# Kernel tuning notes

Hardware: AMD Instinct MI355X
Metric: run time of the kernel (lower is better)

## Reference

```python
import jax, jax.numpy as jnp
import numpy as np

DIM = 512; H = 8; KH = 2; G = 4; DH = 64        # dim, q heads, kv heads, GQA group, head dim
BALL = 128; SEL = 64; TOPK = 2; PDIM = 3        # sliding ball, compress/selection block, topk, pos dim
SCALE = DH ** -0.5


def _rms_norm(x, gamma):
    return x * jax.lax.rsqrt(jnp.mean(x * x, axis=-1, keepdims=True) + 1e-6) * gamma


def _rotary(t):
    # t: (B, h, S, DH); GPT-NeoX style rotate-half rotary embedding
    S = t.shape[-2]
    inv = 1.0 / (10000.0 ** (jnp.arange(0, DH, 2, dtype=jnp.float32) / DH))
    f = jnp.arange(S, dtype=jnp.float32)[:, None] * inv          # (S, DH/2)
    cos = jnp.concatenate([jnp.cos(f), jnp.cos(f)], -1)
    sin = jnp.concatenate([jnp.sin(f), jnp.sin(f)], -1)
    t1, t2 = jnp.split(t, 2, -1)
    return t * cos + jnp.concatenate([-t2, t1], -1) * sin


def _forward(x, pos, pe_w, pe_b, gamma, wq, wk, wv, k_pos, v_pos,
             k_w1, k_b1, k_w2, k_b2, v_w1, v_b1, v_w2, v_b2,
             mem_k, mem_v, w_combine, w_out, num_batches):
    B = num_batches
    # relative position of leaves wrt ball center (no-grad in original)
    p = jax.lax.stop_gradient(pos).reshape(-1, SEL, PDIM)
    rel = (p - p.mean(axis=1, keepdims=True)).reshape(-1, PDIM)
    x = x + rel @ pe_w + pe_b
    x = x.reshape(B, -1, DIM)
    S = x.shape[1]
    nb = S // SEL
    h = _rms_norm(x, gamma)
    q = (h @ wq).reshape(B, S, H, DH).transpose(0, 2, 1, 3)      # (B,H,S,DH)
    k = (h @ wk).reshape(B, S, KH, DH).transpose(0, 2, 1, 3)     # (B,KH,S,DH)
    v = (h @ wv).reshape(B, S, KH, DH).transpose(0, 2, 1, 3)
    qr, kr = _rotary(q), _rotary(k)

    # --- compressed branch: per-block intra-pos emb + MLP compression ---
    kb = k.reshape(B, KH, nb, SEL, DH) + k_pos[None, :, None]
    vb = v.reshape(B, KH, nb, SEL, DH) + v_pos[None, :, None]
    ck = jax.nn.relu(kb.reshape(B, KH, nb, SEL * DH) @ k_w1 + k_b1) @ k_w2 + k_b2
    cv = jax.nn.relu(vb.reshape(B, KH, nb, SEL * DH) @ v_w1 + v_b1) @ v_w2 + v_b2
    ck = jnp.concatenate([jnp.broadcast_to(mem_k[None], (B, KH, 1, DH)), ck], axis=2)
    cv = jnp.concatenate([jnp.broadcast_to(mem_v[None], (B, KH, 1, DH)), cv], axis=2)
    qg = qr.reshape(B, KH, G, S, DH)
    csim = jnp.einsum('bkgsd,bknd->bkgsn', qg, ck) * SCALE
    cattn = jax.nn.softmax(csim, axis=-1)
    cout = jnp.einsum('bkgsn,bknd->bkgsd', cattn, cv).reshape(B, H, S, DH)

    # --- top-k block selection from compressed attention importance ---
    imp = cattn[..., 1:].mean(axis=2)                            # share over grouped q heads: (B,KH,S,nb)
    imp_blk = imp.reshape(B, KH, nb, SEL, nb).mean(axis=3)       # per query block: (B,KH,nb,nb)
    _, sel = jax.lax.top_k(imp_blk, TOPK)                        # (B,KH,nb,TOPK)

    # --- fine branch: each query block attends own + TOPK selected blocks ---
    kblk = kr.reshape(B, KH, nb, SEL, DH)
    vblk = v.reshape(B, KH, nb, SEL, DH)
    gather = jax.vmap(jax.vmap(lambda t, s: t[s]))               # (nb,SEL,DH),(nb,TOPK)->(nb,TOPK,SEL,DH)
    fk = jnp.concatenate([gather(kblk, sel), kblk[:, :, :, None]], axis=3)
    fv = jnp.concatenate([gather(vblk, sel), vblk[:, :, :, None]], axis=3)
    fk = fk.reshape(B, KH, nb, (TOPK + 1) * SEL, DH)
    fv = fv.reshape(B, KH, nb, (TOPK + 1) * SEL, DH)
    qb = qr.reshape(B, KH, G, nb, SEL, DH)
    fsim = jnp.einsum('bkgnqd,bknmd->bkgnqm', qb, fk) * SCALE
    fout = jnp.einsum('bkgnqm,bknmd->bkgnqd', jax.nn.softmax(fsim, -1), fv)
    fout = fout.reshape(B, H, S, DH)

    # --- sliding branch: MiniBallAttn = plain SDPA within balls of size 128 ---
    nw = S // BALL
    qw = qr.reshape(B, H, nw, BALL, DH)
    kw = jnp.repeat(kr, G, axis=1).reshape(B, H, nw, BALL, DH)
    vw = jnp.repeat(v, G, axis=1).reshape(B, H, nw, BALL, DH)
    ssim = jnp.einsum('bhnqd,bhnkd->bhnqk', qw, kw) * SCALE
    sout = jnp.einsum('bhnqk,bhnkd->bhnqd', jax.nn.softmax(ssim, -1), vw)
    sout = sout.reshape(B, H, S, DH)

    # --- sigmoid-gated strategy combine, merge heads, out projection ---
    gates = jax.nn.sigmoid(h @ w_combine).reshape(B, S, H, 3).transpose(0, 2, 1, 3)
    out = gates[..., 0:1] * cout + gates[..., 1:2] * fout + gates[..., 2:3] * sout
    out = out.transpose(0, 2, 1, 3).reshape(B, S, H * DH) @ w_out
    return out.reshape(-1, DIM)


def setup_inputs() -> dict:
    key = jax.random.key(0)
    ks = jax.random.split(key, 16)
    Bn, S = 8, 4096
    N = Bn * S
    CD = SEL * DH
    def lin(k, fi, fo):
        return (jax.random.normal(k, (fi, fo), jnp.float32) / np.sqrt(fi)).astype(jnp.float32)
    return {
        'x': jax.random.normal(ks[0], (N, DIM), jnp.float32),
        'pos': jax.random.normal(ks[1], (N, PDIM), jnp.float32),
        'pe_w': lin(ks[2], PDIM, DIM),
        'pe_b': jnp.zeros((DIM,), jnp.float32),
        'gamma': jnp.ones((DIM,), jnp.float32),
        'wq': lin(ks[3], DIM, H * DH),
        'wk': lin(ks[4], DIM, KH * DH),
        'wv': lin(ks[5], DIM, KH * DH),
        'k_pos': jax.random.normal(ks[6], (KH, SEL, DH), jnp.float32) * 0.02,
        'v_pos': jax.random.normal(ks[7], (KH, SEL, DH), jnp.float32) * 0.02,
        'k_w1': lin(ks[8], CD, CD), 'k_b1': jnp.zeros((CD,), jnp.float32),
        'k_w2': lin(ks[9], CD, DH), 'k_b2': jnp.zeros((DH,), jnp.float32),
        'v_w1': lin(ks[10], CD, CD), 'v_b1': jnp.zeros((CD,), jnp.float32),
        'v_w2': lin(ks[11], CD, DH), 'v_b2': jnp.zeros((DH,), jnp.float32),
        'mem_k': jax.random.normal(ks[12], (KH, 1, DH), jnp.float32) * 0.02,
        'mem_v': jax.random.normal(ks[13], (KH, 1, DH), jnp.float32) * 0.02,
        'w_combine': lin(ks[14], DIM, 3 * H),
        'w_out': lin(ks[15], H * DH, DIM),
        'num_batches': 8,
    }


def reference(x, pos, pe_w, pe_b, gamma, wq, wk, wv, k_pos, v_pos,
              k_w1, k_b1, k_w2, k_b2, v_w1, v_b1, v_w2, v_b2,
              mem_k, mem_v, w_combine, w_out, num_batches):
    return _forward(x, pos, pe_w, pe_b, gamma, wq, wk, wv, k_pos, v_pos,
                    k_w1, k_b1, k_w2, k_b2, v_w1, v_b1, v_w2, v_b2,
                    mem_k, mem_v, w_combine, w_out, num_batches)
```

## Files before the change

kernel.cpp:

```cpp
#include <hip/hip_runtime.h>
#include <stdint.h>

#define DEVI static __device__ __forceinline__
typedef unsigned short u16;
typedef __bf16 bhalf8 __attribute__((ext_vector_type(8)));
typedef float f32x4 __attribute__((ext_vector_type(4)));

DEVI u16 f2bf(float f) {
  union { float f; unsigned u; } v; v.f = f;
  unsigned r = v.u + 0x7FFFu + ((v.u >> 16) & 1u);
  return (u16)(r >> 16);
}
DEVI float bf2f(u16 h) {
  union { unsigned u; float f; } v; v.u = ((unsigned)h) << 16;
  return v.f;
}
DEVI f32x4 MFMA(bhalf8 a, bhalf8 b, f32x4 c) {
  return __builtin_amdgcn_mfma_f32_16x16x32_bf16(a, b, c, 0, 0, 0);
}
DEVI bhalf8 LD8(const u16* p) { return *(const bhalf8*)p; }
DEVI f32x4 zero4() { f32x4 z = {0.f, 0.f, 0.f, 0.f}; return z; }

#define GLDS16(gp, lp) __builtin_amdgcn_global_load_lds( \
    (const __attribute__((address_space(1))) void*)(gp), \
// ... 10 lines not shown
    const float* p = pos + (size_t)(blk * 64 + t) * 3;
    float a = p[0], b = p[1], c = p[2];
#pragma unroll
    for (int o = 32; o; o >>= 1) { a += __shfl_down(a, o); b += __shfl_down(b, o); c += __shfl_down(c, o); }
    if (t == 0) { spm[0] = a * (1.f/64.f); spm[1] = b * (1.f/64.f); spm[2] = c * (1.f/64.f); }
  }
  __syncthreads();
  float r0 = pos[(size_t)n*3+0] - spm[0];
  float r1 = pos[(size_t)n*3+1] - spm[1];
  float r2 = pos[(size_t)n*3+2] - spm[2];
  int c0 = t, c1 = t + 256;
  const float* xr = x + (size_t)n * 512;
  float v0 = xr[c0] + r0*pew[c0] + r1*pew[512+c0] + r2*pew[1024+c0] + peb[c0];
  float v1 = xr[c1] + r0*pew[c1] + r1*pew[512+c1] + r2*pew[1024+c1] + peb[c1];
  float ss = v0*v0 + v1*v1;
#pragma unroll
  for (int o = 32; o; o >>= 1) ss += __shfl_down(ss, o);
  __shared__ float red[4];
  if ((t & 63) == 0) red[t >> 6] = ss;
  __syncthreads();
  float rms = 1.0f / sqrtf((red[0]+red[1]+red[2]+red[3]) * (1.0f/512.0f) + 1e-6f);
  float h0 = v0 * rms * gamma[c0], h1 = v1 * rms * gamma[c1];
  u16 a0 = f2bf(h0); hhi[(size_t)n*512+c0] = a0; hlo[(size_t)n*512+c0] = f2bf(h0 - bf2f(a0));
  u16 a1 = f2bf(h1); hhi[(size_t)n*512+c1] = a1; hlo[(size_t)n*512+c1] = f2bf(h1 - bf2f(a1));
}

__global__ __launch_bounds__(256) void nsa_wcat_rope(const float* __restrict__ wq, const float* __restrict__ wk,
    const float* __restrict__ wv, const float* __restrict__ wc, u16* __restrict__ hi, u16* __restrict__ lo,
    float* __restrict__ ct, float* __restrict__ st) {
  int bidx = blockIdx.x;
  if (bidx < 1792) {
    int idx = bidx * 256 + threadIdx.x;
    int k = idx & 511, n = idx >> 9;
    float v;
    if (n < 512) v = wq[(size_t)k*512 + n];
    else if (n < 640) v = wk[(size_t)k*128 + n - 512];
    else if (n < 768) v = wv[(size_t)k*128 + n - 640];
    else if (n < 792) v = wc[(size_t)k*24 + n - 768];
    else v = 0.f;
    u16 h = f2bf(v); hi[idx] = h; lo[idx] = f2bf(v - bf2f(h));
  } else {
    int idx = (bidx - 1792) * 256 + threadIdx.x;
    int s = idx >> 5, i = idx & 31;
    float e = (float)(2*i) * (1.0f/64.0f);
    float inv = 1.0f / powf(10000.0f, e);
    float f = (float)s * inv;
    ct[idx] = cosf(f); st[idx] = sinf(f);
  }
}

__global__ __launch_bounds__(256) void nsa_vT16(const u16* __restrict__ v16, u16* __restrict__ vT) {
  int blk = blockIdx.x;
  int st = (blk & 63) * 64, bkh = blk >> 6;
  __shared__ u16 tile[64][72];
  int t = threadIdx.x;
  int s = t >> 2, c0 = (t & 3) * 16;
  const u16* src = v16 + ((size_t)bkh*4096 + st + s) * 64;
  *(int4*)&tile[s][c0]   = *(const int4*)&src[c0];
  *(int4*)&tile[s][c0+8] = *(const int4*)&src[c0+8];
  __syncthreads();
  int d = t >> 2, s0 = (t & 3) * 16;
  u16* dst = vT + ((size_t)bkh*64 + d)*4096 + st + s0;
#pragma unroll
  for (int j = 0; j < 16; ++j) dst[j] = tile[s0+j][d];
}

__global__ __launch_bounds__(256) void nsa_wT(const float* __restrict__ src, u16* __restrict__ dhi,
    u16* __restrict__ dlo, int K, int N) {
  __shared__ float tile[64][65];
  int k0 = blockIdx.x * 64, n0 = blockIdx.y * 64;
  int t = threadIdx.x, r = t >> 2, c0 = (t & 3) * 16;
#pragma unroll
  for (int j = 0; j < 16; ++j) tile[r][c0+j] = src[(size_t)(k0+r)*N + n0 + c0 + j];
  __syncthreads();
  size_t ob = (size_t)(n0 + r)*K + k0 + c0;
#pragma unroll
  for (int j = 0; j < 16; ++j) {
    float v = tile[c0+j][r];
    u16 h = f2bf(v); dhi[ob+j] = h;
    if (dlo) dlo[ob+j] = f2bf(v - bf2f(h));
  }
}

__global__ __launch_bounds__(256) void nsa_red_ck(const float* __restrict__ part, const float* __restrict__ mem,
    const float* __restrict__ b2, u16* __restrict__ ckh, u16* __restrict__ ckl) {
  int idx = blockIdx.x * 256 + threadIdx.x;
  if (idx >= 81920) return;
  int d = idx & 63, n = (idx >> 6) % 80, bkh = idx / (80*64);
  int kh = bkh & 1;
  float v;
  if (n == 0) v = mem[kh*64 + d];
  else if (n <= 64) {
    v = b2[d];
    int m = bkh*64 + (n - 1);
#pragma unroll
    for (int kc = 0; kc < 16; ++kc) v += part[((size_t)kc*1024 + m)*64 + d];
  } else v = 0.f;
  u16 h = f2bf(v); ckh[idx] = h; ckl[idx] = f2bf(v - bf2f(h));
}

__global__ __launch_bounds__(256) void nsa_red_cv(const float* __restrict__ part, const float* __restrict__ mem,
    const float* __restrict__ b2, u16* __restrict__ cvT) {
  int idx = blockIdx.x * 256 + threadIdx.x;
  if (idx >= 98304) return;
  int cc = idx % 96, d = (idx / 96) & 63, bkh = idx / (96*64);
  int kh = bkh & 1;
  float v;
  if (cc == 0) v = mem[kh*64 + d];
  else if (cc <= 64) {
    v = b2[d];
    int m = bkh*64 + (cc - 1);
#pragma unroll
    for (int kc = 0; kc < 16; ++kc) v += part[((size_t)kc*1024 + m)*64 + d];
  } else v = 0.f;
  cvT[idx] = f2bf(v);
}

template<bool SPLIT>
__global__ __launch_bounds__(256) void nsa_mlp_fuse(const float* __restrict__ part,
    const float* __restrict__ bias, u16* __restrict__ oh, u16* __restrict__ ol) {
  size_t i = ((size_t)blockIdx.x * 256 + threadIdx.x) * 4;
  int c = (int)(i & 4095);
  float4 a = *(const float4*)&part[i];
  float4 b = *(const float4*)&part[(size_t)4194304 + i];
  float v0 = fmaxf(a.x + b.x + bias[c+0], 0.f);
  float v1 = fmaxf(a.y + b.y + bias[c+1], 0.f);
  float v2 = fmaxf(a.z + b.z + bias[c+2], 0.f);
  float v3 = fmaxf(a.w + b.w + bias[c+3], 0.f);
  u16 h0 = f2bf(v0), h1 = f2bf(v1), h2 = f2bf(v2), h3 = f2bf(v3);
  ((unsigned long long*)oh)[i >> 2] = (unsigned long long)h0 | ((unsigned long long)h1 << 16) |
                                      ((unsigned long long)h2 << 32) | ((unsigned long long)h3 << 48);
  if (SPLIT) {
    u16 l0 = f2bf(v0 - bf2f(h0)), l1 = f2bf(v1 - bf2f(h1));
    u16 l2 = f2bf(v2 - bf2f(h2)), l3 = f2bf(v3 - bf2f(h3));
    ((unsigned long long*)ol)[i >> 2] = (unsigned long long)l0 | ((unsigned long long)l1 << 16) |
                                        ((unsigned long long)l2 << 32) | ((unsigned long long)l3 << 48);
  }
}

__global__ __launch_bounds__(256) void nsa_sentinel(float* __restrict__ o, int n, float val) {
  int i = blockIdx.x * 256 + threadIdx.x;
  if (i < n) o[i] = val;
}

template<bool SPLIT, int EPI, int NOFF = 0>
__global__ __launch_bounds__(256) void nsa_gemm(const u16* __restrict__ Ah, const u16* __restrict__ Al,
    const u16* __restrict__ Bh, const u16* __restrict__ Bl, int K, int N,
    const float* __restrict__ p_cos, float* __restrict__ p_sin,
    u16* __restrict__ out_hi, u16* __restrict__ out_lo, float* __restrict__ og,
    const float* __restrict__ kpos, const float* __restrict__ vpos,
    u16* __restrict__ krb, u16* __restrict__ kbh, u16* __restrict__ kbl,
    u16* __restrict__ v16o, u16* __restrict__ vbh) {
  constexpr int NB = SPLIT ? 4 : 2;
  __shared__ u16 sm[NB * 2 * 4096];
  const int t = threadIdx.x, w = t >> 6, l = t & 63;
  const int wm = w >> 1, wn = w & 1;
  int m0, n0;
  if constexpr (EPI == 0) {
    const int nper = (int)gridDim.y;
    const int bid = blockIdx.y * 256 + blockIdx.x;
    const int xcd = bid & 7, j = bid >> 3;
    const int mg = j / (8*nper), rem = j % (8*nper);
    const int nn = rem >> 3, mi = rem & 7;
    m0 = ((xcd * 4 + mg) * 8 + mi) * 128;
    n0 = (nn + NOFF) * 128;
  } else {
    const int MBn = gridDim.x;
    const int nwg = MBn * gridDim.y;
    const int bid = blockIdx.y * MBn + blockIdx.x;
    const int swz = (bid & 7) * (nwg >> 3) + (bid >> 3);
    m0 = (swz % MBn) * 128; n0 = (swz / MBn) * 128;
  }
  const int klen = K / (int)gridDim.z;
  const int kb0 = blockIdx.z * klen;
  const int row = l & 15;
  const int kc8 = ((l >> 4) ^ ((l >> 1) & 3)) * 8;
  const int gsc = ((l & 3) ^ ((l >> 3) & 3)) * 8;
  const int sr = l >> 2;
  f32x4 acc[4][4];
#pragma unroll
  for (int a = 0; a < 4; ++a)
#pragma unroll
    for (int b = 0; b < 4; ++b) acc[a][b] = zero4();

  auto STAGE = [&](int buf, int k0) {
    u16* base = sm + buf * NB * 4096;
#pragma unroll
    for (int s2 = 0; s2 < 2; ++s2) {
      int seg = w*2 + s2;
      int r = seg*16 + sr;
      size_t ga = (size_t)(m0 + r)*K + k0 + gsc;
      size_t gb = (size_t)(n0 + r)*K + k0 + gsc;
      GLDS16(&Ah[ga], base + seg*512);
      GLDS16(&Bh[gb], base + 4096 + seg*512);
      if (SPLIT) {
        GLDS16(&Al[ga], base + 2*4096 + seg*512);
        GLDS16(&Bl[gb], base + 3*4096 + seg*512);
      }
    }
  };

  const int nt = klen >> 5;
  STAGE(0, kb0);
  __syncthreads();
  int cur = 0;
  for (int kt = 0; kt < nt; ++kt) {
    if (kt + 1 < nt) STAGE(cur ^ 1, kb0 + (kt + 1) * 32);
    u16* bA  = sm + cur * NB * 4096;
    u16* bB  = bA + 4096;
    u16* bAl = bA + 2*4096;
    u16* bBl = bA + 3*4096;
    bhalf8 af[4], afl[4];
#pragma unroll
    for (int mf = 0; mf < 4; ++mf) {
      af[mf] = LD8(&bA[(wm*64 + mf*16 + row)*32 + kc8]);
      if (SPLIT) afl[mf] = LD8(&bAl[(wm*64 + mf*16 + row)*32 + kc8]);
    }
#pragma unroll
    for (int nf = 0; nf < 4; ++nf) {
      bhalf8 bfh = LD8(&bB[(wn*64 + nf*16 + row)*32 + kc8]);
      bhalf8 bfl;
      if (SPLIT) bfl = LD8(&bBl[(wn*64 + nf*16 + row)*32 + kc8]);
#pragma unroll
      for (int mf = 0; mf < 4; ++mf) {
        acc[mf][nf] = MFMA(af[mf], bfh, acc[mf][nf]);
        if (SPLIT) {
          acc[mf][nf] = MFMA(af[mf], bfl, acc[mf][nf]);
          acc[mf][nf] = MFMA(afl[mf], bfh, acc[mf][nf]);
        }
      }
    }
    __syncthreads();
    cur ^= 1;
  }
  if constexpr (EPI == 0) {
    if (n0 < 512) {
#pragma unroll
      for (int mf = 0; mf < 4; ++mf)
#pragma unroll
        for (int i = 0; i < 4; ++i) {
          int r = m0 + wm*64 + mf*16 + (l >> 4)*4 + i;
          int s = r & 4095, b = r >> 12;
#pragma unroll
          for (int nf = 0; nf < 2; ++nf) {
            int c = n0 + wn*64 + nf*16 + (l & 15);
            int hq = c >> 6, dd = c & 31;
            float t1 = acc[mf][nf][i], t2 = acc[mf][nf+2][i];
            float cs = p_cos[s*32 + dd], sn = p_sin[s*32 + dd];
            float o1 = t1*cs - t2*sn, o2 = t2*cs + t1*sn;
            size_t ob = (((size_t)(b*8 + hq))*4096 + s)*64;
            u16 h1 = f2bf(o1); out_hi[ob+dd] = h1;    out_lo[ob+dd] = f2bf(o1 - bf2f(h1));
            u16 h2 = f2bf(o2); out_hi[ob+dd+32] = h2; out_lo[ob+dd+32] = f2bf(o2 - bf2f(h2));
          }
        }
    } else if (n0 == 512) {
      int kh = wn;
#pragma unroll
      for (int mf = 0; mf < 4; ++mf)
#pragma unroll
        for (int i = 0; i < 4; ++i) {
          int r = m0 + wm*64 + mf*16 + (l >> 4)*4 + i;
          int s = r & 4095, b = r >> 12;
          int n = s >> 6, sl = s & 63;
          size_t krbase = ((size_t)(b*2 + kh)*4096 + s)*64;
          size_t kbbase = ((size_t)(b*128 + kh*64 + n))*4096 + sl*64;
#pragma unroll
          for (int nf = 0; nf < 2; ++nf) {
            int dd = nf*16 + (l & 15);
            float t1 = acc[mf][nf][i], t2 = acc[mf][nf+2][i];
            float cs = p_cos[s*32 + dd], sn = p_sin[s*32 + dd];
            krb[krbase + dd]      = f2bf(t1*cs - t2*sn);
            krb[krbase + dd + 32] = f2bf(t2*cs + t1*sn);
          }
#pragma unroll
          for (int nf = 0; nf < 4; ++nf) {
            int dk = nf*16 + (l & 15);
            float v = acc[mf][nf][i] + kpos[(kh*64 + sl)*64 + dk];
            u16 h = f2bf(v);
            kbh[kbbase + dk] = h;
            kbl[kbbase + dk] = f2bf(v - bf2f(h));
          }
        }
    } else if (n0 == 640) {
      int kh = wn;
#pragma unroll
      for (int mf = 0; mf < 4; ++mf)
#pragma unroll
        for (int i = 0; i < 4; ++i) {
          int r = m0 + wm*64 + mf*16 + (l >> 4)*4 + i;
          int s = r & 4095, b = r >> 12;
          int n = s >> 6, sl = s & 63;
          size_t v16base = ((size_t)(b*2 + kh)*4096 + s)*64;
          size_t vbbase = ((size_t)(b*128 + kh*64 + n))*4096 + sl*64;
#pragma unroll
          for (int nf = 0; nf < 4; ++nf) {
            int dv = nf*16 + (l & 15);
            float vv = acc[mf][nf][i];
            v16o[v16base + dv] = f2bf(vv);
            vbh[vbbase + dv] = f2bf(vv + vpos[(kh*64 + sl)*64 + dv]);
          }
        }
    } else {
#pragma unroll
      for (int mf = 0; mf < 4; ++mf)
#pragma unroll
        for (int nf = 0; nf < 4; ++nf)
#pragma unroll
          for (int i = 0; i < 4; ++i) {
            int r = m0 + wm*64 + mf*16 + (l >> 4)*4 + i;
            int c = n0 + wn*64 + nf*16 + (l & 15);
            if (c < 792) og[(size_t)r*24 + (c - 768)] = 1.0f / (1.0f + expf(-acc[mf][nf][i]));
          }
    }
  } else if constexpr (EPI == 2) {
#pragma unroll
    for (int mf = 0; mf < 4; ++mf)
#pragma unroll
      for (int nf = 0; nf < 4; ++nf)
#pragma unroll
        for (int i = 0; i < 4; ++i) {
          int r = m0 + wm*64 + mf*16 + (l >> 4)*4 + i;
          int c = n0 + wn*64 + nf*16 + (l & 15);
          p_sin[(size_t)r*N + c] = acc[mf][nf][i];
        }
  } else {
    const int M = (int)gridDim.x * 128;
#pragma unroll
    for (int mf = 0; mf < 4; ++mf)
#pragma unroll
      for (int nf = 0; nf < 4; ++nf)
#pragma unroll
        for (int i = 0; i < 4; ++i) {
          int r = m0 + wm*64 + mf*16 + (l >> 4)*4 + i;
          int c = n0 + wn*64 + nf*16 + (l & 15);
          p_sin[((size_t)blockIdx.z * M + r) * (size_t)N + c] = acc[mf][nf][i];
        }
  }
}

template<bool SPLIT>
__global__ __launch_bounds__(256) void nsa_gemm64(const u16* __restrict__ Ah, const u16* __restrict__ Al,
    const u16* __restrict__ Bh, const u16* __restrict__ Bl, float* __restrict__ part) {
  constexpr int NB = SPLIT ? 4 : 2;
  __shared__ u16 sm[NB * 2 * 2048];
  const int t = threadIdx.x, w = t >> 6, l = t & 63;
  const int mt = blockIdx.x, kc = blockIdx.y;
  const int row = l & 15;
  const int kc8 = ((l >> 4) ^ ((l >> 1) & 3)) * 8;
  const int gsc = ((l & 3) ^ ((l >> 3) & 3)) * 8;
  const int sr = l >> 2;
  f32x4 acc[4];
#pragma unroll
  for (int a = 0; a < 4; ++a) acc[a] = zero4();

  auto STAGE = [&](int buf, int k0) {
    u16* base = sm + buf * NB * 2048;
    int r = w*16 + sr;
    size_t ga = (size_t)(mt*64 + r)*4096 + k0 + gsc;
    size_t gb = (size_t)r*4096 + k0 + gsc;
    GLDS16(&Ah[ga], base + w*512);
    GLDS16(&Bh[gb], base + 2048 + w*512);
    if (SPLIT) {
      GLDS16(&Al[ga], base + 2*2048 + w*512);
      GLDS16(&Bl[gb], base + 3*2048 + w*512);
    }
  };

  STAGE(0, kc*256);
  __syncthreads();
  int cur = 0;
  for (int kt = 0; kt < 8; ++kt) {
    if (kt + 1 < 8) STAGE(cur ^ 1, kc*256 + (kt + 1) * 32);
    u16* bA  = sm + cur * NB * 2048;
    u16* bB  = bA + 2048;
    u16* bAl = bA + 2*2048;
    u16* bBl = bA + 3*2048;
    bhalf8 a = LD8(&bA[(w*16 + row)*32 + kc8]);
    bhalf8 al;
    if (SPLIT) al = LD8(&bAl[(w*16 + row)*32 + kc8]);
#pragma unroll
    for (int nf = 0; nf < 4; ++nf) {
      bhalf8 b = LD8(&bB[(nf*16 + row)*32 + kc8]);
      bhalf8 bl;
      if (SPLIT) bl = LD8(&bBl[(nf*16 + row)*32 + kc8]);
      acc[nf] = MFMA(a, b, acc[nf]);
      if (SPLIT) {
        acc[nf] = MFMA(a, bl, acc[nf]);
        acc[nf] = MFMA(al, b, acc[nf]);
      }
    }
    __syncthreads();
    cur ^= 1;
  }
#pragma unroll
  for (int nf = 0; nf < 4; ++nf)
#pragma unroll
    for (int i = 0; i < 4; ++i) {
      int m = mt*64 + w*16 + (l >> 4)*4 + i;
      int d = nf*16 + (l & 15);
      part[((size_t)kc*1024 + m)*64 + d] = acc[nf][i];
    }
}


__global__ __launch_bounds__(256) void nsa_attn_comp(const u16* __restrict__ qrh, const u16* __restrict__ qrl,
    const u16* __restrict__ ckh, const u16* __restrict__ ckl, const u16* __restrict__ cvT,
    const float* __restrict__ g32, u16* __restrict__ comb, float* __restrict__ imp) {
  __shared__ u16 smem[24832];
  __shared__ float sImp[4 * 80];
  u16* sKh = smem;
  u16* sKl = smem + 5760;
  u16* sVT = smem + 11520;
  u16* sP  = smem + 18176;
  const int t = threadIdx.x, w = t >> 6, l = t & 63;
  const int bid = blockIdx.x;
  const int qt = bid & 63, kh = (bid >> 6) & 1, b = bid >> 7;
  const int row = l & 15, kg = (l >> 4) * 8;
  size_t kbase = (size_t)(b*2 + kh) * 80 * 64;
  size_t vbase = (size_t)(b*2 + kh) * 64 * 96;
  for (int e = t; e < 640; e += 256) {
    int r = e >> 3, c = (e & 7) * 8;
    *(int4*)&sKh[r*72 + c] = *(const int4*)&ckh[kbase + r*64 + c];
    *(int4*)&sKl[r*72 + c] = *(const int4*)&ckl[kbase + r*64 + c];
  }
  for (int e = t; e < 768; e += 256) {
    int r = e / 12, ch = e % 12;
    *(int4*)&sVT[r*104 + ch*8] = *(const int4*)&cvT[vbase + (size_t)r*96 + ch*8];
  }
  for (int e = l; e < 80; e += 64) sImp[w*80 + e] = 0.f;
#pragma unroll
  for (int i = 0; i < 4; ++i)
    sP[(w*16 + (l & 15))*104 + 80 + (l >> 4)*4 + i] = 0;
  __syncthreads();
  for (int g = 0; g < 4; ++g) {
    size_t qbase = ((size_t)((b*2 + kh)*4 + g)*4096 + qt*64) * 64 + (size_t)(w*16 + row)*64;
    bhalf8 ah0 = LD8(&qrh[qbase + kg]);
    bhalf8 ah1 = LD8(&qrh[qbase + 32 + kg]);
    bhalf8 al0 = LD8(&qrl[qbase + kg]);
    bhalf8 al1 = LD8(&qrl[qbase + 32 + kg]);
    f32x4 sc[5];
#pragma unroll
    for (int nf = 0; nf < 5; ++nf) sc[nf] = zero4();
#pragma unroll
    for (int kk = 0; kk < 2; ++kk) {
      bhalf8 ah = kk ? ah1 : ah0;
      bhalf8 al = kk ? al1 : al0;
#pragma unroll
      for (int nf = 0; nf < 5; ++nf) {
        bhalf8 bh = LD8(&sKh[(nf*16 + row)*72 + kk*32 + kg]);
        bhalf8 bl = LD8(&sKl[(nf*16 + row)*72 + kk*32 + kg]);
        sc[nf] = MFMA(ah, bh, sc[nf]);
        sc[nf] = MFMA(ah, bl, sc[nf]);
        sc[nf] = MFMA(al, bh, sc[nf]);
      }
    }
    float mx[4] = {-1e30f, -1e30f, -1e30f, -1e30f};
#pragma unroll
    for (int nf = 0; nf < 5; ++nf)
#pragma unroll
      for (int i = 0; i < 4; ++i) {
        int col = nf*16 + (l & 15);
        float v = (col < 65) ? sc[nf][i] * 0.125f : -1e30f;
        sc[nf][i] = v;
        mx[i] = fmaxf(mx[i], v);
      }
#pragma unroll
    for (int i = 0; i < 4; ++i)
#pragma unroll
      for (int o = 1; o < 16; o <<= 1) mx[i] = fmaxf(mx[i], __shfl_xor(mx[i], o));
    float sum[4] = {0.f, 0.f, 0.f, 0.f};
#pragma unroll
    for (int nf = 0; nf < 5; ++nf)
#pragma unroll
      for (int i = 0; i < 4; ++i) {
        int col = nf*16 + (l & 15);
        float p = (col < 65) ? expf(sc[nf][i] - mx[i]) : 0.f;
        sc[nf][i] = p;
        sum[i] += p;
      }
#pragma unroll
    for (int i = 0; i < 4; ++i)
#pragma unroll
      for (int o = 1; o < 16; o <<= 1) sum[i] += __shfl_xor(sum[i], o);
// ... 223 lines not shown
#pragma unroll
      for (int i = 0; i < 4; ++i)
#pragma unroll
        for (int o = 1; o < 16; o <<= 1) mx[i] = fmaxf(mx[i], __shfl_xor(mx[i], o));
      float sum[4] = {0.f, 0.f, 0.f, 0.f};
#pragma unroll
      for (int nf = 0; nf < 8; ++nf)
#pragma unroll
        for (int i = 0; i < 4; ++i) {
          float p = expf(sc[nf][i] - mx[i]);
          sc[nf][i] = p;
          sum[i] += p;
        }
#pragma unroll
      for (int i = 0; i < 4; ++i)
#pragma unroll
        for (int o = 1; o < 16; o <<= 1) sum[i] += __shfl_xor(sum[i], o);
      float inv[4];
#pragma unroll
      for (int i = 0; i < 4; ++i) inv[i] = 1.0f / sum[i];
#pragma unroll
      for (int nf = 0; nf < 8; ++nf)
#pragma unroll
        for (int i = 0; i < 4; ++i)
          sP[(w*16 + (l >> 4)*4 + i)*136 + nf*16 + (l & 15)] = f2bf(sc[nf][i] * inv[i]);
      f32x4 ovv[4];
#pragma unroll
      for (int nf = 0; nf < 4; ++nf) ovv[nf] = zero4();
#pragma unroll
      for (int kk = 0; kk < 4; ++kk) {
        bhalf8 a = LD8(&sP[(w*16 + row)*136 + kk*32 + kg]);
#pragma unroll
        for (int nf = 0; nf < 4; ++nf) {
          bhalf8 bv = LD8(&sVT[(nf*16 + row)*136 + kk*32 + kg]);
          ovv[nf] = MFMA(a, bv, ovv[nf]);
        }
      }
#pragma unroll
      for (int i = 0; i < 4; ++i) {
        int q = qt*64 + w*16 + (l >> 4)*4 + i;
        float gate = g32[((size_t)b*4096 + q)*24 + hh*3 + 2];
#pragma unroll
        for (int nf = 0; nf < 4; ++nf) {
          int d = nf*16 + (l & 15);
          size_t oi = (((size_t)b*4096 + q)*8 + hh)*64 + d;
          comb[oi] = f2bf(bf2f(comb[oi]) + gate * ovv[nf][i]);
        }
      }
    }
  }
}


extern "C" void kernel_launch(void* const* d_in, const int* in_sizes, int n_in,
                              void* d_out, int out_size, void* d_ws, size_t ws_size,
                              hipStream_t stream) {
  const float* x     = (const float*)d_in[0];
  const float* pos   = (const float*)d_in[1];
  const float* pe_w  = (const float*)d_in[2];
  const float* pe_b  = (const float*)d_in[3];
  const float* gamma = (const float*)d_in[4];
  const float* wq    = (const float*)d_in[5];
  const float* wk    = (const float*)d_in[6];
  const float* wv    = (const float*)d_in[7];
  const float* k_pos = (const float*)d_in[8];
  const float* v_pos = (const float*)d_in[9];
  const float* k_w1  = (const float*)d_in[10];
  const float* k_b1  = (const float*)d_in[11];
  const float* k_w2  = (const float*)d_in[12];
  const float* k_b2  = (const float*)d_in[13];
  const float* v_w1  = (const float*)d_in[14];
  const float* v_b1  = (const float*)d_in[15];
  const float* v_w2  = (const float*)d_in[16];
  const float* v_b2  = (const float*)d_in[17];
  const float* mem_k = (const float*)d_in[18];
  const float* mem_v = (const float*)d_in[19];
  const float* w_cmb = (const float*)d_in[20];
  const float* w_out = (const float*)d_in[21];
  float* out = (float*)d_out;
  char* ws = (char*)d_ws;

  size_t off = 0;
  auto A = [&](size_t b) { size_t o = off; off += (b + 255) & ~(size_t)255; return o; };
  const size_t oR1 = A(67108864);
  const size_t oR2 = A(67108864);
  const size_t oR4 = A(16777216);
  const size_t oR5 = A(16777216);
  const size_t oR6 = A(16777216);
  const size_t oR7 = A(16777216);
  const size_t oR8 = A(3145728);
  const size_t oR9 = A(2097152);
  const size_t o_cos = A(524288),  o_sin = A(524288);
  const size_t o_ckh = A(163840),  o_ckl = A(163840);
  const size_t o_cvT = A(196608);
  const size_t o_woh = A(524288),  o_wol = A(524288);
  const size_t o_imp = A(262144);
  const size_t o_sel = A(8192);
  const size_t o_part = A(4194304);
  const size_t o_part1 = A(33554432);

  if (ws_size < off) {
    nsa_sentinel<<<(out_size + 255)/256, 256, 0, stream>>>(out, out_size, (float)(ws_size >> 20));
    return;
  }

#define WP(T, o) ((T*)(ws + (o)))
  u16*  h_hi = WP(u16, oR1);           u16* h_lo = WP(u16, oR1 + 33554432);
  u16*  w1h  = WP(u16, oR1);           u16* w1l  = WP(u16, oR1 + 33554432);
  u16*  combp = WP(u16, oR1);
  u16*  qrh  = WP(u16, oR2);           u16* qrl  = WP(u16, oR2 + 33554432);
  u16*  th   = WP(u16, oR4);           u16* tl   = WP(u16, oR4 + 8388608);
  u16*  v16b = WP(u16, oR5);           u16* vbh  = WP(u16, oR5 + 8388608);
  u16*  kbh  = WP(u16, oR6);           u16* kbl  = WP(u16, oR6 + 8388608);
  u16*  krb  = WP(u16, oR7);           u16* vTb  = WP(u16, oR7 + 8388608);
  float* g32 = WP(float, oR8);
  u16*  wch  = WP(u16, oR9);           u16* wcl  = WP(u16, oR9 + 917504);
  u16*  w2h  = WP(u16, oR9);           u16* w2l  = WP(u16, oR9 + 524288);
  u16*  w2vh = WP(u16, oR9 + 1048576); u16* w2vl = WP(u16, oR9 + 1572864);
  float* cosb = WP(float, o_cos);      float* sinb = WP(float, o_sin);
  u16*  ckh  = WP(u16, o_ckh);         u16* ckl  = WP(u16, o_ckl);
  u16*  cvT  = WP(u16, o_cvT);
  u16*  woh  = WP(u16, o_woh);         u16* wol  = WP(u16, o_wol);
  float* imp = WP(float, o_imp);
  int*  selp = WP(int, o_sel);
  float* part = WP(float, o_part);
  float* part1 = WP(float, o_part1);

  nsa_hnorm<<<32768, 256, 0, stream>>>(x, pos, pe_w, pe_b, gamma, h_hi, h_lo);
  nsa_wcat_rope<<<2304, 256, 0, stream>>>(wq, wk, wv, w_cmb, wch, wcl, cosb, sinb);
  nsa_gemm<true, 0, 0><<<dim3(256, 5, 1), 256, 0, stream>>>(h_hi, h_lo, wch, wcl, 512, 896,
      cosb, sinb, qrh, qrl, g32, k_pos, v_pos, krb, kbh, kbl, v16b, vbh);
  nsa_gemm<false, 0, 5><<<dim3(256, 2, 1), 256, 0, stream>>>(h_hi, nullptr, wch, nullptr, 512, 896,
      cosb, sinb, qrh, qrl, g32, k_pos, v_pos, krb, kbh, kbl, v16b, vbh);
  nsa_vT16<<<1024, 256, 0, stream>>>(v16b, vTb);
  nsa_wT<<<dim3(64, 64), 256, 0, stream>>>(k_w1, w1h, w1l, 4096, 4096);
  nsa_gemm<true, 3><<<dim3(8, 32, 2), 256, 0, stream>>>(kbh, kbl, w1h, w1l, 4096, 4096,
      nullptr, part1, nullptr, nullptr, nullptr, nullptr, nullptr, nullptr, nullptr, nullptr,
      nullptr, nullptr);
  nsa_mlp_fuse<true><<<4096, 256, 0, stream>>>(part1, k_b1, th, tl);
  nsa_wT<<<dim3(64, 1), 256, 0, stream>>>(k_w2, w2h, w2l, 4096, 64);
  nsa_gemm64<true><<<dim3(16, 16), 256, 0, stream>>>(th, tl, w2h, w2l, part);
  nsa_red_ck<<<320, 256, 0, stream>>>(part, mem_k, k_b2, ckh, ckl);
  nsa_wT<<<dim3(64, 64), 256, 0, stream>>>(v_w1, w1h, nullptr, 4096, 4096);
  nsa_gemm<false, 3><<<dim3(8, 32, 2), 256, 0, stream>>>(vbh, nullptr, w1h, nullptr, 4096, 4096,
      nullptr, part1, nullptr, nullptr, nullptr, nullptr, nullptr, nullptr, nullptr, nullptr,
      nullptr, nullptr);
  nsa_mlp_fuse<false><<<4096, 256, 0, stream>>>(part1, v_b1, th, nullptr);
  nsa_wT<<<dim3(64, 1), 256, 0, stream>>>(v_w2, w2vh, nullptr, 4096, 64);
  nsa_gemm64<false><<<dim3(16, 16), 256, 0, stream>>>(th, nullptr, w2vh, nullptr, part);
  nsa_red_cv<<<384, 256, 0, stream>>>(part, mem_v, v_b2, cvT);
  nsa_attn_comp<<<1024, 256, 0, stream>>>(qrh, qrl, ckh, ckl, cvT, g32, combp, imp);
  nsa_top2<<<1024, 64, 0, stream>>>(imp, selp);
  nsa_attn_fine<<<1024, 256, 0, stream>>>(qrh, krb, vTb, selp, g32, combp);
  nsa_attn_slide<<<512, 256, 0, stream>>>(qrh, krb, vTb, g32, combp);
  nsa_wT<<<dim3(8, 8), 256, 0, stream>>>(w_out, woh, nullptr, 512, 512);
  nsa_gemm<false, 2><<<dim3(256, 4, 1), 256, 0, stream>>>(combp, nullptr, woh, nullptr, 512, 512,
      nullptr, out, nullptr, nullptr, nullptr, nullptr, nullptr, nullptr, nullptr, nullptr,
      nullptr, nullptr);
#undef WP
}
```

Baseline: 723.6 us.

## Merge K/V compression MLP GEMMs into combined launches with fused bias-ReLU epilogue

The K and V compression MLP paths now share one kernel each for the first GEMM, the second GEMM, the weight transposes and the final reduction, instead of running as separate serial launches. The first-layer GEMM drops its split-K partial buffer and applies bias, ReLU and bf16 hi/lo conversion in its epilogue, which removes the separate mlp_fuse pass and its fp32 traffic. The QKV projection becomes a single launch that picks split precision per N-tile at runtime. In exchange, the merged first GEMM has no split-K, so each block runs 128 k-steps over 512 blocks. K blocks do three MFMAs per step and V blocks one, which can leave the load unbalanced.

```diff
diff --git a/kernel.cpp b/kernel.cpp
--- a/kernel.cpp
+++ b/kernel.cpp
@@ -116,59 +116,58 @@
   }
 }
 
-__global__ __launch_bounds__(256) void nsa_red_ck(const float* __restrict__ part, const float* __restrict__ mem,
-    const float* __restrict__ b2, u16* __restrict__ ckh, u16* __restrict__ ckl) {
+__global__ __launch_bounds__(256) void nsa_wT2(const float* __restrict__ srcA, u16* __restrict__ dhA,
+    u16* __restrict__ dlA, const float* __restrict__ srcB, u16* __restrict__ dhB, u16* __restrict__ dlB,
+    int K, int N) {
+  const float* src = blockIdx.z ? srcB : srcA;
+  u16* dhi = blockIdx.z ? dhB : dhA;
+  u16* dlo = blockIdx.z ? dlB : dlA;
+  __shared__ float tile[64][65];
+  int k0 = blockIdx.x * 64, n0 = blockIdx.y * 64;
+  int t = threadIdx.x, r = t >> 2, c0 = (t & 3) * 16;
+#pragma unroll
+  for (int j = 0; j < 16; ++j) tile[r][c0+j] = src[(size_t)(k0+r)*N + n0 + c0 + j];
+  __syncthreads();
+  size_t ob = (size_t)(n0 + r)*K + k0 + c0;
+#pragma unroll
+  for (int j = 0; j < 16; ++j) {
+    float v = tile[c0+j][r];
+    u16 h = f2bf(v); dhi[ob+j] = h;
+    if (dlo) dlo[ob+j] = f2bf(v - bf2f(h));
+  }
+}
+
+__global__ __launch_bounds__(256) void nsa_red_ckcv(const float* __restrict__ part,
+    const float* __restrict__ mem_k, const float* __restrict__ kb2,
+    const float* __restrict__ mem_v, const float* __restrict__ vb2,
+    u16* __restrict__ ckh, u16* __restrict__ ckl, u16* __restrict__ cvT) {
   int idx = blockIdx.x * 256 + threadIdx.x;
-  if (idx >= 81920) return;
-  int d = idx & 63, n = (idx >> 6) % 80, bkh = idx / (80*64);
-  int kh = bkh & 1;
-  float v;
-  if (n == 0) v = mem[kh*64 + d];
-  else if (n <= 64) {
-    v = b2[d];
-    int m = bkh*64 + (n - 1);
-#pragma unroll
-    for (int kc = 0; kc < 16; ++kc) v += part[((size_t)kc*1024 + m)*64 + d];
-  } else v = 0.f;
-  u16 h = f2bf(v); ckh[idx] = h; ckl[idx] = f2bf(v - bf2f(h));
-}
-
-__global__ __launch_bounds__(256) void nsa_red_cv(const float* __restrict__ part, const float* __restrict__ mem,
-    const float* __restrict__ b2, u16* __restrict__ cvT) {
-  int idx = blockIdx.x * 256 + threadIdx.x;
-  if (idx >= 98304) return;
-  int cc = idx % 96, d = (idx / 96) & 63, bkh = idx / (96*64);
-  int kh = bkh & 1;
-  float v;
-  if (cc == 0) v = mem[kh*64 + d];
-  else if (cc <= 64) {
-    v = b2[d];
-    int m = bkh*64 + (cc - 1);
-#pragma unroll
-    for (int kc = 0; kc < 16; ++kc) v += part[((size_t)kc*1024 + m)*64 + d];
-  } else v = 0.f;
-  cvT[idx] = f2bf(v);
-}
-
-template<bool SPLIT>
-__global__ __launch_bounds__(256) void nsa_mlp_fuse(const float* __restrict__ part,
-    const float* __restrict__ bias, u16* __restrict__ oh, u16* __restrict__ ol) {
-  size_t i = ((size_t)blockIdx.x * 256 + threadIdx.x) * 4;
-  int c = (int)(i & 4095);
-  float4 a = *(const float4*)&part[i];
-  float4 b = *(const float4*)&part[(size_t)4194304 + i];
-  float v0 = fmaxf(a.x + b.x + bias[c+0], 0.f);
-  float v1 = fmaxf(a.y + b.y + bias[c+1], 0.f);
-  float v2 = fmaxf(a.z + b.z + bias[c+2], 0.f);
-  float v3 = fmaxf(a.w + b.w + bias[c+3], 0.f);
-  u16 h0 = f2bf(v0), h1 = f2bf(v1), h2 = f2bf(v2), h3 = f2bf(v3);
-  ((unsigned long long*)oh)[i >> 2] = (unsigned long long)h0 | ((unsigned long long)h1 << 16) |
-                                      ((unsigned long long)h2 << 32) | ((unsigned long long)h3 << 48);
-  if (SPLIT) {
-    u16 l0 = f2bf(v0 - bf2f(h0)), l1 = f2bf(v1 - bf2f(h1));
-    u16 l2 = f2bf(v2 - bf2f(h2)), l3 = f2bf(v3 - bf2f(h3));
-    ((unsigned long long*)ol)[i >> 2] = (unsigned long long)l0 | ((unsigned long long)l1 << 16) |
-                                        ((unsigned long long)l2 << 32) | ((unsigned long long)l3 << 48);
+  if (idx < 81920) {
+    int d = idx & 63, n = (idx >> 6) % 80, bkh = idx / (80*64);
+    int kh = bkh & 1;
+    float v;
+    if (n == 0) v = mem_k[kh*64 + d];
+    else if (n <= 64) {
+      v = kb2[d];
+      int m = bkh*64 + (n - 1);
+#pragma unroll
+      for (int kc = 0; kc < 16; ++kc) v += part[((size_t)kc*1024 + m)*64 + d];
+    } else v = 0.f;
+    u16 h = f2bf(v); ckh[idx] = h; ckl[idx] = f2bf(v - bf2f(h));
+  } else if (idx < 81920 + 98304) {
+    int j = idx - 81920;
+    int cc = j % 96, d = (j / 96) & 63, bkh = j / (96*64);
+    int kh = bkh & 1;
+    const float* pv = part + (size_t)16*1024*64;
+    float v;
+    if (cc == 0) v = mem_v[kh*64 + d];
+    else if (cc <= 64) {
+      v = vb2[d];
+      int m = bkh*64 + (cc - 1);
+#pragma unroll
+      for (int kc = 0; kc < 16; ++kc) v += pv[((size_t)kc*1024 + m)*64 + d];
+    } else v = 0.f;
+    cvT[j] = f2bf(v);
   }
 }
 
@@ -177,7 +176,7 @@
   if (i < n) o[i] = val;
 }
 
-template<bool SPLIT, int EPI, int NOFF = 0>
+template<bool SPLIT, int EPI>
 __global__ __launch_bounds__(256) void nsa_gemm(const u16* __restrict__ Ah, const u16* __restrict__ Al,
     const u16* __restrict__ Bh, const u16* __restrict__ Bl, int K, int N,
     const float* __restrict__ p_cos, float* __restrict__ p_sin,
@@ -197,7 +196,7 @@
     const int mg = j / (8*nper), rem = j % (8*nper);
     const int nn = rem >> 3, mi = rem & 7;
     m0 = ((xcd * 4 + mg) * 8 + mi) * 128;
-    n0 = (nn + NOFF) * 128;
+    n0 = nn * 128;
   } else {
     const int MBn = gridDim.x;
     const int nwg = MBn * gridDim.y;
@@ -205,8 +204,7 @@
     const int swz = (bid & 7) * (nwg >> 3) + (bid >> 3);
     m0 = (swz % MBn) * 128; n0 = (swz / MBn) * 128;
   }
-  const int klen = K / (int)gridDim.z;
-  const int kb0 = blockIdx.z * klen;
+  const bool dsp = SPLIT && (EPI != 0 || n0 <= 512);
   const int row = l & 15;
   const int kc8 = ((l >> 4) ^ ((l >> 1) & 3)) * 8;
   const int gsc = ((l & 3) ^ ((l >> 3) & 3)) * 8;
@@ -227,19 +225,19 @@
       size_t gb = (size_t)(n0 + r)*K + k0 + gsc;
       GLDS16(&Ah[ga], base + seg*512);
       GLDS16(&Bh[gb], base + 4096 + seg*512);
-      if (SPLIT) {
+      if (SPLIT && dsp) {
         GLDS16(&Al[ga], base + 2*4096 + seg*512);
         GLDS16(&Bl[gb], base + 3*4096 + seg*512);
       }
     }
   };
 
-  const int nt = klen >> 5;
-  STAGE(0, kb0);
+  const int nt = K >> 5;
+  STAGE(0, 0);
   __syncthreads();
   int cur = 0;
   for (int kt = 0; kt < nt; ++kt) {
-    if (kt + 1 < nt) STAGE(cur ^ 1, kb0 + (kt + 1) * 32);
+    if (kt + 1 < nt) STAGE(cur ^ 1, (kt + 1) * 32);
     u16* bA  = sm + cur * NB * 4096;
     u16* bB  = bA + 4096;
     u16* bAl = bA + 2*4096;
@@ -248,17 +246,17 @@
 #pragma unroll
     for (int mf = 0; mf < 4; ++mf) {
       af[mf] = LD8(&bA[(wm*64 + mf*16 + row)*32 + kc8]);
-      if (SPLIT) afl[mf] = LD8(&bAl[(wm*64 + mf*16 + row)*32 + kc8]);
+      if (dsp) afl[mf] = LD8(&bAl[(wm*64 + mf*16 + row)*32 + kc8]);
     }
 #pragma unroll
     for (int nf = 0; nf < 4; ++nf) {
       bhalf8 bfh = LD8(&bB[(wn*64 + nf*16 + row)*32 + kc8]);
       bhalf8 bfl;
-      if (SPLIT) bfl = LD8(&bBl[(wn*64 + nf*16 + row)*32 + kc8]);
+      if (dsp) bfl = LD8(&bBl[(wn*64 + nf*16 + row)*32 + kc8]);
 #pragma unroll
       for (int mf = 0; mf < 4; ++mf) {
         acc[mf][nf] = MFMA(af[mf], bfh, acc[mf][nf]);
-        if (SPLIT) {
+        if (dsp) {
           acc[mf][nf] = MFMA(af[mf], bfl, acc[mf][nf]);
           acc[mf][nf] = MFMA(afl[mf], bfh, acc[mf][nf]);
         }
@@ -346,7 +344,7 @@
             if (c < 792) og[(size_t)r*24 + (c - 768)] = 1.0f / (1.0f + expf(-acc[mf][nf][i]));
           }
     }
-  } else if constexpr (EPI == 2) {
+  } else {
 #pragma unroll
     for (int mf = 0; mf < 4; ++mf)
 #pragma unroll
@@ -357,28 +355,115 @@
           int c = n0 + wn*64 + nf*16 + (l & 15);
           p_sin[(size_t)r*N + c] = acc[mf][nf][i];
         }
-  } else {
-    const int M = (int)gridDim.x * 128;
-#pragma unroll
-    for (int mf = 0; mf < 4; ++mf)
-#pragma unroll
-      for (int nf = 0; nf < 4; ++nf)
-#pragma unroll
-        for (int i = 0; i < 4; ++i) {
-          int r = m0 + wm*64 + mf*16 + (l >> 4)*4 + i;
-          int c = n0 + wn*64 + nf*16 + (l & 15);
-          p_sin[((size_t)blockIdx.z * M + r) * (size_t)N + c] = acc[mf][nf][i];
-        }
-  }
-}
-
-template<bool SPLIT>
-__global__ __launch_bounds__(256) void nsa_gemm64(const u16* __restrict__ Ah, const u16* __restrict__ Al,
-    const u16* __restrict__ Bh, const u16* __restrict__ Bl, float* __restrict__ part) {
-  constexpr int NB = SPLIT ? 4 : 2;
-  __shared__ u16 sm[NB * 2 * 2048];
+  }
+}
+
+__global__ __launch_bounds__(256) void nsa_mlp1(const u16* __restrict__ kbh, const u16* __restrict__ kbl,
+    const u16* __restrict__ vbh, const u16* __restrict__ w1kh, const u16* __restrict__ w1kl,
+    const u16* __restrict__ w1vh, const float* __restrict__ kb1, const float* __restrict__ vb1,
+    u16* __restrict__ th, u16* __restrict__ tl, u16* __restrict__ tv) {
+  __shared__ u16 sm[4 * 2 * 4096];
   const int t = threadIdx.x, w = t >> 6, l = t & 63;
-  const int mt = blockIdx.x, kc = blockIdx.y;
+  const int wm = w >> 1, wn = w & 1;
+  const int bid = blockIdx.x;
+  const int xcd = bid & 7, u = bid >> 3;
+  const bool isK = u < 32;
+  const int uu = isK ? u : u - 32;
+  const int m0 = (uu & 7) * 128;
+  const int n0 = (xcd * 4 + (uu >> 3)) * 128;
+  const u16* Ah = isK ? kbh : vbh;
+  const u16* Bh = isK ? w1kh : w1vh;
+  constexpr int K = 4096;
+  const int row = l & 15;
+  const int kc8 = ((l >> 4) ^ ((l >> 1) & 3)) * 8;
+  const int gsc = ((l & 3) ^ ((l >> 3) & 3)) * 8;
+  const int sr = l >> 2;
+  f32x4 acc[4][4];
+#pragma unroll
+  for (int a = 0; a < 4; ++a)
+#pragma unroll
+    for (int b = 0; b < 4; ++b) acc[a][b] = zero4();
+
+  auto STAGE = [&](int buf, int k0) {
+    u16* base = sm + buf * 4 * 4096;
+#pragma unroll
+    for (int s2 = 0; s2 < 2; ++s2) {
+      int seg = w*2 + s2;
+      int r = seg*16 + sr;
+      size_t ga = (size_t)(m0 + r)*K + k0 + gsc;
+      size_t gb = (size_t)(n0 + r)*K + k0 + gsc;
+      GLDS16(&Ah[ga], base + seg*512);
+      GLDS16(&Bh[gb], base + 4096 + seg*512);
+      if (isK) {
+        GLDS16(&kbl[ga], base + 2*4096 + seg*512);
+        GLDS16(&w1kl[gb], base + 3*4096 + seg*512);
+      }
+    }
+  };
+
+  STAGE(0, 0);
+  __syncthreads();
+  int cur = 0;
+  for (int kt = 0; kt < 128; ++kt) {
+    if (kt + 1 < 128) STAGE(cur ^ 1, (kt + 1) * 32);
+    u16* bA  = sm + cur * 4 * 4096;
+    u16* bB  = bA + 4096;
+    u16* bAl = bA + 2*4096;
+    u16* bBl = bA + 3*4096;
+    bhalf8 af[4], afl[4];
+#pragma unroll
+    for (int mf = 0; mf < 4; ++mf) {
+      af[mf] = LD8(&bA[(wm*64 + mf*16 + row)*32 + kc8]);
+      if (isK) afl[mf] = LD8(&bAl[(wm*64 + mf*16 + row)*32 + kc8]);
+    }
+#pragma unroll
+    for (int nf = 0; nf < 4; ++nf) {
+      bhalf8 bfh = LD8(&bB[(wn*64 + nf*16 + row)*32 + kc8]);
+      bhalf8 bfl;
+      if (isK) bfl = LD8(&bBl[(wn*64 + nf*16 + row)*32 + kc8]);
+#pragma unroll
+      for (int mf = 0; mf < 4; ++mf) {
+        acc[mf][nf] = MFMA(af[mf], bfh, acc[mf][nf]);
+        if (isK) {
+          acc[mf][nf] = MFMA(af[mf], bfl, acc[mf][nf]);
+          acc[mf][nf] = MFMA(afl[mf], bfh, acc[mf][nf]);
+        }
+      }
+    }
+    __syncthreads();
+    cur ^= 1;
+  }
+  const float* bias = isK ? kb1 : vb1;
+#pragma unroll
+  for (int mf = 0; mf < 4; ++mf)
+#pragma unroll
+    for (int nf = 0; nf < 4; ++nf)
+#pragma unroll
+      for (int i = 0; i < 4; ++i) {
+        int r = m0 + wm*64 + mf*16 + (l >> 4)*4 + i;
+        int c = n0 + wn*64 + nf*16 + (l & 15);
+        float v = fmaxf(acc[mf][nf][i] + bias[c], 0.f);
+        if (isK) {
+          u16 h = f2bf(v);
+          th[(size_t)r*4096 + c] = h;
+          tl[(size_t)r*4096 + c] = f2bf(v - bf2f(h));
+        } else {
+          tv[(size_t)r*4096 + c] = f2bf(v);
+        }
+      }
+}
+
+__global__ __launch_bounds__(256) void nsa_gemm64m(const u16* __restrict__ th, const u16* __restrict__ tl,
+    const u16* __restrict__ tv, const u16* __restrict__ w2h, const u16* __restrict__ w2l,
+    const u16* __restrict__ w2vh, float* __restrict__ part) {
+  __shared__ u16 sm[4 * 2 * 2048];
+  const int t = threadIdx.x, w = t >> 6, l = t & 63;
+  const int mt = blockIdx.x;
+  const bool isK = blockIdx.y < 16;
+  const int kc = blockIdx.y & 15;
+  const u16* Ah = isK ? th : tv;
+  const u16* Bh = isK ? w2h : w2vh;
+  float* po = part + (isK ? 0 : (size_t)16*1024*64);
   const int row = l & 15;
   const int kc8 = ((l >> 4) ^ ((l >> 1) & 3)) * 8;
   const int gsc = ((l & 3) ^ ((l >> 3) & 3)) * 8;
@@ -388,15 +473,15 @@
   for (int a = 0; a < 4; ++a) acc[a] = zero4();
 
   auto STAGE = [&](int buf, int k0) {
-    u16* base = sm + buf * NB * 2048;
+    u16* base = sm + buf * 4 * 2048;
     int r = w*16 + sr;
     size_t ga = (size_t)(mt*64 + r)*4096 + k0 + gsc;
     size_t gb = (size_t)r*4096 + k0 + gsc;
     GLDS16(&Ah[ga], base + w*512);
     GLDS16(&Bh[gb], base + 2048 + w*512);
-    if (SPLIT) {
-      GLDS16(&Al[ga], base + 2*2048 + w*512);
-      GLDS16(&Bl[gb], base + 3*2048 + w*512);
+    if (isK) {
+      GLDS16(&tl[ga], base + 2*2048 + w*512);
+      GLDS16(&w2l[gb], base + 3*2048 + w*512);
     }
   };
 
@@ -405,20 +490,20 @@
   int cur = 0;
   for (int kt = 0; kt < 8; ++kt) {
     if (kt + 1 < 8) STAGE(cur ^ 1, kc*256 + (kt + 1) * 32);
-    u16* bA  = sm + cur * NB * 2048;
+    u16* bA  = sm + cur * 4 * 2048;
     u16* bB  = bA + 2048;
     u16* bAl = bA + 2*2048;
     u16* bBl = bA + 3*2048;
     bhalf8 a = LD8(&bA[(w*16 + row)*32 + kc8]);
     bhalf8 al;
-    if (SPLIT) al = LD8(&bAl[(w*16 + row)*32 + kc8]);
+    if (isK) al = LD8(&bAl[(w*16 + row)*32 + kc8]);
 #pragma unroll
     for (int nf = 0; nf < 4; ++nf) {
       bhalf8 b = LD8(&bB[(nf*16 + row)*32 + kc8]);
       bhalf8 bl;
-      if (SPLIT) bl = LD8(&bBl[(nf*16 + row)*32 + kc8]);
+      if (isK) bl = LD8(&bBl[(nf*16 + row)*32 + kc8]);
       acc[nf] = MFMA(a, b, acc[nf]);
-      if (SPLIT) {
+      if (isK) {
         acc[nf] = MFMA(a, bl, acc[nf]);
         acc[nf] = MFMA(al, b, acc[nf]);
       }
@@ -432,7 +517,7 @@
     for (int i = 0; i < 4; ++i) {
       int m = mt*64 + w*16 + (l >> 4)*4 + i;
       int d = nf*16 + (l & 15);
-      part[((size_t)kc*1024 + m)*64 + d] = acc[nf][i];
+      po[((size_t)kc*1024 + m)*64 + d] = acc[nf][i];
     }
 }
 
@@ -822,7 +907,7 @@
 
   size_t off = 0;
   auto A = [&](size_t b) { size_t o = off; off += (b + 255) & ~(size_t)255; return o; };
-  const size_t oR1 = A(67108864);
+  const size_t oR1 = A(100663296);
   const size_t oR2 = A(67108864);
   const size_t oR4 = A(16777216);
   const size_t oR5 = A(16777216);
@@ -833,11 +918,10 @@
   const size_t o_cos = A(524288),  o_sin = A(524288);
   const size_t o_ckh = A(163840),  o_ckl = A(163840);
   const size_t o_cvT = A(196608);
-  const size_t o_woh = A(524288),  o_wol = A(524288);
+  const size_t o_woh = A(524288);
   const size_t o_imp = A(262144);
   const size_t o_sel = A(8192);
-  const size_t o_part = A(4194304);
-  const size_t o_part1 = A(33554432);
+  const size_t o_part = A(8388608);
 
   if (ws_size < off) {
     nsa_sentinel<<<(out_size + 255)/256, 256, 0, stream>>>(out, out_size, (float)(ws_size >> 20));
@@ -846,49 +930,37 @@
 
 #define WP(T, o) ((T*)(ws + (o)))
   u16*  h_hi = WP(u16, oR1);           u16* h_lo = WP(u16, oR1 + 33554432);
-  u16*  w1h  = WP(u16, oR1);           u16* w1l  = WP(u16, oR1 + 33554432);
+  u16*  w1kh = WP(u16, oR1);           u16* w1kl = WP(u16, oR1 + 33554432);
+  u16*  w1vh = WP(u16, oR1 + 67108864);
   u16*  combp = WP(u16, oR1);
   u16*  qrh  = WP(u16, oR2);           u16* qrl  = WP(u16, oR2 + 33554432);
   u16*  th   = WP(u16, oR4);           u16* tl   = WP(u16, oR4 + 8388608);
   u16*  v16b = WP(u16, oR5);           u16* vbh  = WP(u16, oR5 + 8388608);
+  u16*  tv   = WP(u16, oR5);
   u16*  kbh  = WP(u16, oR6);           u16* kbl  = WP(u16, oR6 + 8388608);
   u16*  krb  = WP(u16, oR7);           u16* vTb  = WP(u16, oR7 + 8388608);
   float* g32 = WP(float, oR8);
   u16*  wch  = WP(u16, oR9);           u16* wcl  = WP(u16, oR9 + 917504);
   u16*  w2h  = WP(u16, oR9);           u16* w2l  = WP(u16, oR9 + 524288);
-  u16*  w2vh = WP(u16, oR9 + 1048576); u16* w2vl = WP(u16, oR9 + 1572864);
+  u16*  w2vh = WP(u16, oR9 + 1048576);
   float* cosb = WP(float, o_cos);      float* sinb = WP(float, o_sin);
   u16*  ckh  = WP(u16, o_ckh);         u16* ckl  = WP(u16, o_ckl);
   u16*  cvT  = WP(u16, o_cvT);
-  u16*  woh  = WP(u16, o_woh);         u16* wol  = WP(u16, o_wol);
+  u16*  woh  = WP(u16, o_woh);
   float* imp = WP(float, o_imp);
   int*  selp = WP(int, o_sel);
   float* part = WP(float, o_part);
-  float* part1 = WP(float, o_part1);
 
   nsa_hnorm<<<32768, 256, 0, stream>>>(x, pos, pe_w, pe_b, gamma, h_hi, h_lo);
   nsa_wcat_rope<<<2304, 256, 0, stream>>>(wq, wk, wv, w_cmb, wch, wcl, cosb, sinb);
-  nsa_gemm<true, 0, 0><<<dim3(256, 5, 1), 256, 0, stream>>>(h_hi, h_lo, wch, wcl, 512, 896,
-      cosb, sinb, qrh, qrl, g32, k_pos, v_pos, krb, kbh, kbl, v16b, vbh);
-  nsa_gemm<false, 0, 5><<<dim3(256, 2, 1), 256, 0, stream>>>(h_hi, nullptr, wch, nullptr, 512, 896,
+  nsa_gemm<true, 0><<<dim3(256, 7, 1), 256, 0, stream>>>(h_hi, h_lo, wch, wcl, 512, 896,
       cosb, sinb, qrh, qrl, g32, k_pos, v_pos, krb, kbh, kbl, v16b, vbh);
   nsa_vT16<<<1024, 256, 0, stream>>>(v16b, vTb);
-  nsa_wT<<<dim3(64, 64), 256, 0, stream>>>(k_w1, w1h, w1l, 4096, 4096);
-  nsa_gemm<true, 3><<<dim3(8, 32, 2), 256, 0, stream>>>(kbh, kbl, w1h, w1l, 4096, 4096,
-      nullptr, part1, nullptr, nullptr, nullptr, nullptr, nullptr, nullptr, nullptr, nullptr,
-      nullptr, nullptr);
-  nsa_mlp_fuse<true><<<4096, 256, 0, stream>>>(part1, k_b1, th, tl);
-  nsa_wT<<<dim3(64, 1), 256, 0, stream>>>(k_w2, w2h, w2l, 4096, 64);
-  nsa_gemm64<true><<<dim3(16, 16), 256, 0, stream>>>(th, tl, w2h, w2l, part);
-  nsa_red_ck<<<320, 256, 0, stream>>>(part, mem_k, k_b2, ckh, ckl);
-  nsa_wT<<<dim3(64, 64), 256, 0, stream>>>(v_w1, w1h, nullptr, 4096, 4096);
-  nsa_gemm<false, 3><<<dim3(8, 32, 2), 256, 0, stream>>>(vbh, nullptr, w1h, nullptr, 4096, 4096,
-      nullptr, part1, nullptr, nullptr, nullptr, nullptr, nullptr, nullptr, nullptr, nullptr,
-      nullptr, nullptr);
-  nsa_mlp_fuse<false><<<4096, 256, 0, stream>>>(part1, v_b1, th, nullptr);
-  nsa_wT<<<dim3(64, 1), 256, 0, stream>>>(v_w2, w2vh, nullptr, 4096, 64);
-  nsa_gemm64<false><<<dim3(16, 16), 256, 0, stream>>>(th, nullptr, w2vh, nullptr, part);
-  nsa_red_cv<<<384, 256, 0, stream>>>(part, mem_v, v_b2, cvT);
+  nsa_wT2<<<dim3(64, 64, 2), 256, 0, stream>>>(k_w1, w1kh, w1kl, v_w1, w1vh, nullptr, 4096, 4096);
+  nsa_wT2<<<dim3(64, 1, 2), 256, 0, stream>>>(k_w2, w2h, w2l, v_w2, w2vh, nullptr, 4096, 64);
+  nsa_mlp1<<<512, 256, 0, stream>>>(kbh, kbl, vbh, w1kh, w1kl, w1vh, k_b1, v_b1, th, tl, tv);
+  nsa_gemm64m<<<dim3(16, 32), 256, 0, stream>>>(th, tl, tv, w2h, w2l, w2vh, part);
+  nsa_red_ckcv<<<704, 256, 0, stream>>>(part, mem_k, k_b2, mem_v, v_b2, ckh, ckl, cvT);
   nsa_attn_comp<<<1024, 256, 0, stream>>>(qrh, qrl, ckh, ckl, cvT, g32, combp, imp);
   nsa_top2<<<1024, 64, 0, stream>>>(imp, selp);
   nsa_attn_fine<<<1024, 256, 0, stream>>>(qrh, krb, vTb, selp, g32, combp);
```

Measured after the change: 694.1 us. 4.1% less time.
